# Kernel tuning notes

Hardware: AMD Instinct MI355X
Metric: run time of the kernel (lower is better)

The kernel has to match this reference:

```python
import jax, jax.numpy as jnp
import numpy as np

D_MODEL = 1024
NUM_HEADS = 16
D_K = D_MODEL // NUM_HEADS
B, S = 4, 2048


def setup_inputs() -> dict:
    key = jax.random.key(0)
    ks = jax.random.split(key, 11)
    scale = 1.0 / np.sqrt(D_MODEL)
    inp = {
        "query": jax.random.normal(ks[0], (B, S, D_MODEL), dtype=jnp.float32),
        "key": jax.random.normal(ks[1], (B, S, D_MODEL), dtype=jnp.float32),
        "value": jax.random.normal(ks[2], (B, S, D_MODEL), dtype=jnp.float32),
        "w_q": jax.random.normal(ks[3], (D_MODEL, D_MODEL), dtype=jnp.float32) * scale,
        "b_q": jnp.zeros((D_MODEL,), dtype=jnp.float32),
        "w_k": jax.random.normal(ks[4], (D_MODEL, D_MODEL), dtype=jnp.float32) * scale,
        "b_k": jnp.zeros((D_MODEL,), dtype=jnp.float32),
        "w_v": jax.random.normal(ks[5], (D_MODEL, D_MODEL), dtype=jnp.float32) * scale,
        "b_v": jnp.zeros((D_MODEL,), dtype=jnp.float32),
        "w_o": jax.random.normal(ks[6], (D_MODEL, D_MODEL), dtype=jnp.float32) * scale,
        "b_o": jnp.zeros((D_MODEL,), dtype=jnp.float32),
    }
    return inp


def reference(query, key, value, w_q, b_q, w_k, b_k, w_v, b_v, w_o, b_o):
    # Linear projections; torch Linear computes x @ W.T + b, here w_* stored as (out, in)
    def proj(x, w, b):
        y = jnp.einsum("bsd,ed->bse", x, w) + b
        # [B, S, D] -> [B, H, S, d_k]
        return y.reshape(B, S, NUM_HEADS, D_K).transpose(0, 2, 1, 3)

    Q = proj(query, w_q, b_q)
    K = proj(key, w_k, b_k)
    V = proj(value, w_v, b_v)

    scores = jnp.einsum("bhqd,bhkd->bhqk", Q, K) / jnp.sqrt(jnp.float32(D_K))
    weights = jax.nn.softmax(scores, axis=-1)
    attn = jnp.einsum("bhqk,bhkd->bhqd", weights, V)  # [B, H, S, d_k]
    attn = attn.transpose(0, 2, 1, 3).reshape(B, S, D_MODEL)
    return jnp.einsum("bsd,ed->bse", attn, w_o) + b_o
```

## Files before the change

kernel.cpp:

```cpp
#include <hip/hip_runtime.h>
#include <hip/hip_bf16.h>

#define D_MODEL 1024
#define NHEADS 16
#define DKH 64
#define BATCH 4
#define SEQ 2048
#define MROWS (BATCH*SEQ)
#define BSD ((size_t)MROWS * D_MODEL)
#define WSZ ((size_t)D_MODEL * D_MODEL)
#define LOG2E 1.4426950408889634f
#define NT (SEQ/64)

typedef __attribute__((ext_vector_type(8)))  short   s16x8;
typedef __attribute__((ext_vector_type(8)))  __bf16  bf16x8;
typedef __attribute__((ext_vector_type(4)))  __bf16  bf16x4;
typedef __attribute__((ext_vector_type(4)))  float   f32x4;
typedef __attribute__((ext_vector_type(16))) float   f32x16;

#define SWZ(row, scol) ((((int)(row)) << 6) + (((int)(scol)) ^ ((((int)(row)) & 7) << 3)))

__device__ inline short f2bf(float f) {
    __bf16 h = (__bf16)f;
    short s; __builtin_memcpy(&s, &h, 2); return s;
}

__device__ inline unsigned pk2(float a, float b) {
    unsigned r;
    asm("v_cvt_pk_bf16_f32 %0, %1, %2" : "=v"(r) : "v"(a), "v"(b));
    return r;
}
__device__ inline bf16x8 mk8(unsigned w0, unsigned w1, unsigned w2, unsigned w3) {
    union { unsigned u[4]; bf16x8 v; } x;
    x.u[0] = w0; x.u[1] = w1; x.u[2] = w2; x.u[3] = w3;
    return x.v;
}

__device__ inline void gl_lds16(const void* g, void* l) {
    __builtin_amdgcn_global_load_lds(
        (const __attribute__((address_space(1))) unsigned*)g,
        (__attribute__((address_space(3))) unsigned*)l, 16, 0, 0);
}

struct CvtPtrs { const float* src[7]; short* dst[7]; };

__global__ __launch_bounds__(256) void cvt_all(CvtPtrs p)
{
    const int bx = blockIdx.x;
    int buf, boff;
    if (bx < 3 * 4096) { buf = bx >> 12; boff = bx & 4095; }
    else { const int r = bx - 3 * 4096; buf = 3 + (r >> 9); boff = r & 511; }
    const float* __restrict__ src = p.src[buf];
    short* __restrict__ dst = p.dst[buf];
    const size_t i = ((size_t)boff * 256 + threadIdx.x) * 8;
    const float4 a = *(const float4*)(src + i);
    const float4 b = *(const float4*)(src + i + 4);
    s16x8 v;
    v[0]=f2bf(a.x); v[1]=f2bf(a.y); v[2]=f2bf(a.z); v[3]=f2bf(a.w);
    v[4]=f2bf(b.x); v[5]=f2bf(b.y); v[6]=f2bf(b.z); v[7]=f2bf(b.w);
    *(s16x8*)(dst + i) = v;
}

template<int OMODE>
__device__ __forceinline__ void gemm_body(
    const short* __restrict__ A, const short* __restrict__ W,
    const float* __restrict__ bias, void* __restrict__ Cout, float scale)
{
    __shared__ __align__(16) short As[128 * 64];
    __shared__ __align__(16) short Bs[128 * 64];
    const int t   = threadIdx.x;
    const int l   = t & 63;
    const int wid = t >> 6;
    const int g   = l >> 4, r16 = l & 15;
    const int wm  = wid >> 1, wn = wid & 1;
    const int bid = blockIdx.x + (blockIdx.y << 3);
    const int swz = (bid & 7) * 64 + (bid >> 3);
    const int n0  = (swz & 7) * 128, m0 = (swz >> 3) * 128;
    const int srow = t >> 3;
    const int scol = (t & 7) * 8;

    f32x4 acc[4][4];
    #pragma unroll
    for (int mi = 0; mi < 4; ++mi)
        #pragma unroll
        for (int ni = 0; ni < 4; ++ni)
            acc[mi][ni] = (f32x4)0.0f;

    const short* Ap = A + (size_t)(m0 + srow) * D_MODEL + scol;
    const short* Wp = W + (size_t)(n0 + srow) * D_MODEL + scol;
    short* AsW = As + wid * 512;
    short* BsW = Bs + wid * 512;

    for (int k0 = 0; k0 < D_MODEL; k0 += 64) {
        #pragma unroll
        for (int p = 0; p < 4; ++p) {
            gl_lds16(Ap + (size_t)p * 32 * D_MODEL + k0, AsW + p * 2048);
            gl_lds16(Wp + (size_t)p * 32 * D_MODEL + k0, BsW + p * 2048);
        }
        __syncthreads();
        #pragma unroll
        for (int kc = 0; kc < 2; ++kc) {
            bf16x8 a[4], b[4];
            #pragma unroll
            for (int mi = 0; mi < 4; ++mi)
                a[mi] = *(const bf16x8*)&As[(wm * 64 + mi * 16 + r16) * 64 + kc * 32 + g * 8];
            #pragma unroll
            for (int ni = 0; ni < 4; ++ni)
                b[ni] = *(const bf16x8*)&Bs[(wn * 64 + ni * 16 + r16) * 64 + kc * 32 + g * 8];
            #pragma unroll
            for (int mi = 0; mi < 4; ++mi)
                #pragma unroll
                for (int ni = 0; ni < 4; ++ni)
                    acc[mi][ni] = __builtin_amdgcn_mfma_f32_16x16x32_bf16(a[mi], b[ni], acc[mi][ni], 0, 0, 0);
        }
        __syncthreads();
    }

    #pragma unroll
    for (int mi = 0; mi < 4; ++mi)
        #pragma unroll
        for (int ni = 0; ni < 4; ++ni)
            #pragma unroll
            for (int j = 0; j < 4; ++j) {
                const int m = m0 + wm * 64 + mi * 16 + g * 4 + j;
                const int n = n0 + wn * 64 + ni * 16 + r16;
                float v = acc[mi][ni][j] + bias[n];
                if (OMODE == 1) {
                    v *= scale;
                    const size_t idx = (((size_t)((m >> 11) * NHEADS + (n >> 6)) << 11)
                                        + (size_t)(m & 2047)) * DKH + (n & 63);
                    ((short*)Cout)[idx] = f2bf(v);
                } else {
                    ((float*)Cout)[(size_t)m * D_MODEL + n] = v;
                }
            }
}

struct QkvArgs {
    const short* A[3]; const short* W[3]; const float* bias[3];
    short* out[3]; float scale[3];
};

__global__ __launch_bounds__(256, 2) void gemm_qkv(QkvArgs q) {
    const int z = blockIdx.z;
    gemm_body<1>(q.A[z], q.W[z], q.bias[z], q.out[z], q.scale[z]);
}

__global__ __launch_bounds__(256, 2) void gemm_out(
    const short* A, const short* W, const float* bias, float* C) {
    gemm_body<0>(A, W, bias, C, 1.0f);
}

__global__ __launch_bounds__(256) void transpose_v(
    const short* __restrict__ Vb, short* __restrict__ Vt)
{
    __shared__ __align__(16) short T[64][72];
    const int t  = threadIdx.x;
    const int bh = blockIdx.y;
    const int s0 = blockIdx.x * 64;
    const int row = t >> 2, cb = (t & 3) * 16;
    const short* src = Vb + ((size_t)bh * SEQ + s0 + row) * DKH + cb;
    *(s16x8*)&T[row][cb]     = *(const s16x8*)(src);
    *(s16x8*)&T[row][cb + 8] = *(const s16x8*)(src + 8);
    __syncthreads();
    const int d = t >> 2, sb = (t & 3) * 16;
    s16x8 o0, o1;
    #pragma unroll
    for (int j = 0; j < 8; ++j) { o0[j] = T[sb + j][d]; o1[j] = T[sb + 8 + j][d]; }
    short* dst = Vt + ((size_t)bh * DKH + d) * SEQ + s0 + sb;
    *(s16x8*)(dst)     = o0;
    *(s16x8*)(dst + 8) = o1;
}

__global__ __launch_bounds__(256, 3) void attn_mfma(
    const short* __restrict__ Qg, const short* __restrict__ Kg,
    const short* __restrict__ Vtg, short* __restrict__ Ab)
{
    __shared__ __align__(16) short lds[16384];
    const int t   = threadIdx.x;
    const int l   = t & 63;
    const int wid = t >> 6;
    const int l31 = l & 31, hi = l >> 5;
    const int bid = blockIdx.x + (blockIdx.y << 4);
    const int swz = (bid & 7) * 128 + (bid >> 3);
    const int bh  = swz >> 4, b = bh >> 4, h = bh & 15;
    const int q0  = (swz & 15) << 7;
    const int wq0 = wid * 32;
    const int srow = t >> 3, scol = (t & 7) * 8;
    const int kr = t >> 2, kcb = (t & 3) * 16;

    #pragma unroll
    for (int p = 0; p < 4; ++p) {
        const int row = srow + p * 32;
        *(s16x8*)&lds[SWZ(row, scol)] =
            *(const s16x8*)&Qg[((size_t)bh * SEQ + q0 + row) * DKH + scol];
    }
    const short* Kbase = Kg  + (size_t)bh * SEQ * DKH;
    const short* Vbase = Vtg + (size_t)bh * DKH * SEQ;
    s16x8 kpf0 = *(const s16x8*)&Kbase[(size_t)kr * DKH + kcb];
    s16x8 kpf1 = *(const s16x8*)&Kbase[(size_t)kr * DKH + kcb + 8];
    s16x8 vpf0 = *(const s16x8*)&Vbase[(size_t)kr * SEQ + kcb];
    s16x8 vpf1 = *(const s16x8*)&Vbase[(size_t)kr * SEQ + kcb + 8];
    __syncthreads();

    bf16x8 bq[4];
    #pragma unroll
    for (int kc = 0; kc < 4; ++kc)
        bq[kc] = *(const bf16x8*)&lds[SWZ(wq0 + l31, kc * 16 + hi * 8)];

    *(s16x8*)&lds[8192  + SWZ(kr, kcb)]     = kpf0;
    *(s16x8*)&lds[8192  + SWZ(kr, kcb + 8)] = kpf1;
    *(s16x8*)&lds[12288 + SWZ(kr, kcb)]     = vpf0;
    *(s16x8*)&lds[12288 + SWZ(kr, kcb + 8)] = vpf1;
    kpf0 = *(const s16x8*)&Kbase[(size_t)(64 + kr) * DKH + kcb];
    kpf1 = *(const s16x8*)&Kbase[(size_t)(64 + kr) * DKH + kcb + 8];
    vpf0 = *(const s16x8*)&Vbase[(size_t)kr * SEQ + 64 + kcb];
    vpf1 = *(const s16x8*)&Vbase[(size_t)kr * SEQ + 64 + kcb + 8];
    __syncthreads();

    f32x16 o0 = (f32x16)0.0f, o1 = (f32x16)0.0f;
    float m_r = -1e30f, l_r = 0.0f;

    for (int kt = 0; kt < NT; ++kt) {
        const int cur = kt & 1;
        const int KO = cur ? 0     : 8192;
        const int VO = cur ? 4096  : 12288;
        const int KN = cur ? 8192  : 0;
        const int VN = cur ? 12288 : 4096;
        if (kt + 1 < NT) {
            *(s16x8*)&lds[KN + SWZ(kr, kcb)]     = kpf0;
            *(s16x8*)&lds[KN + SWZ(kr, kcb + 8)] = kpf1;
            *(s16x8*)&lds[VN + SWZ(kr, kcb)]     = vpf0;
            *(s16x8*)&lds[VN + SWZ(kr, kcb + 8)] = vpf1;
        }
        if (kt + 2 < NT) {
            kpf0 = *(const s16x8*)&Kbase[(size_t)((kt + 2) * 64 + kr) * DKH + kcb];
            kpf1 = *(const s16x8*)&Kbase[(size_t)((kt + 2) * 64 + kr) * DKH + kcb + 8];
            vpf0 = *(const s16x8*)&Vbase[(size_t)kr * SEQ + (kt + 2) * 64 + kcb];
            vpf1 = *(const s16x8*)&Vbase[(size_t)kr * SEQ + (kt + 2) * 64 + kcb + 8];
        }

        f32x16 s0 = (f32x16)0.0f, s1 = (f32x16)0.0f;
        __builtin_amdgcn_s_setprio(1);
        #pragma unroll
        for (int kc = 0; kc < 4; ++kc) {
            const bf16x8 ak0 = *(const bf16x8*)&lds[KO + SWZ(l31,      kc * 16 + hi * 8)];
            const bf16x8 ak1 = *(const bf16x8*)&lds[KO + SWZ(32 + l31, kc * 16 + hi * 8)];
            s0 = __builtin_amdgcn_mfma_f32_32x32x16_bf16(ak0, bq[kc], s0, 0, 0, 0);
            s1 = __builtin_amdgcn_mfma_f32_32x32x16_bf16(ak1, bq[kc], s1, 0, 0, 0);
        }
        __builtin_amdgcn_s_setprio(0);

        float mx = s0[0];
        #pragma unroll
        for (int r = 1; r < 16; ++r) mx = fmaxf(mx, s0[r]);
        #pragma unroll
        for (int r = 0; r < 16; ++r) mx = fmaxf(mx, s1[r]);
        mx = fmaxf(mx, __shfl_xor(mx, 32));
        if (__any(mx > m_r + 8.0f)) {
            const float mnew = fmaxf(m_r, mx);
            const float resc = __builtin_amdgcn_exp2f(m_r - mnew);
            m_r = mnew;
            l_r *= resc;
            #pragma unroll
            for (int r = 0; r < 16; ++r) { o0[r] *= resc; o1[r] *= resc; }
        }
        float sum = 0.0f;
        #pragma unroll
        for (int r = 0; r < 16; ++r) {
            const float p = __builtin_amdgcn_exp2f(s0[r] - m_r);
            s0[r] = p; sum += p;
        }
        #pragma unroll
        for (int r = 0; r < 16; ++r) {
            const float p = __builtin_amdgcn_exp2f(s1[r] - m_r);
            s1[r] = p; sum += p;
        }
        l_r += sum;

        bf16x8 bp[4];
        {
            unsigned a0 = pk2(s0[0], s0[1]),  b0 = pk2(s0[4],  s0[5]);
            unsigned a1 = pk2(s0[2], s0[3]),  b1 = pk2(s0[6],  s0[7]);
            asm("v_permlane32_swap_b32 %0, %1" : "+v"(a0), "+v"(b0));
            asm("v_permlane32_swap_b32 %0, %1" : "+v"(a1), "+v"(b1));
            bp[0] = mk8(a0, a1, b0, b1);
            unsigned a2 = pk2(s0[8], s0[9]),   b2 = pk2(s0[12], s0[13]);
            unsigned a3 = pk2(s0[10], s0[11]), b3 = pk2(s0[14], s0[15]);
            asm("v_permlane32_swap_b32 %0, %1" : "+v"(a2), "+v"(b2));
            asm("v_permlane32_swap_b32 %0, %1" : "+v"(a3), "+v"(b3));
            bp[1] = mk8(a2, a3, b2, b3);
        }
        {
            unsigned a0 = pk2(s1[0], s1[1]),  b0 = pk2(s1[4],  s1[5]);
            unsigned a1 = pk2(s1[2], s1[3]),  b1 = pk2(s1[6],  s1[7]);
            asm("v_permlane32_swap_b32 %0, %1" : "+v"(a0), "+v"(b0));
            asm("v_permlane32_swap_b32 %0, %1" : "+v"(a1), "+v"(b1));
            bp[2] = mk8(a0, a1, b0, b1);
            unsigned a2 = pk2(s1[8], s1[9]),   b2 = pk2(s1[12], s1[13]);
            unsigned a3 = pk2(s1[10], s1[11]), b3 = pk2(s1[14], s1[15]);
            asm("v_permlane32_swap_b32 %0, %1" : "+v"(a2), "+v"(b2));
            asm("v_permlane32_swap_b32 %0, %1" : "+v"(a3), "+v"(b3));
            bp[3] = mk8(a2, a3, b2, b3);
        }

        __builtin_amdgcn_s_setprio(1);
        #pragma unroll
        for (int ks = 0; ks < 4; ++ks) {
            const bf16x8 av0 = *(const bf16x8*)&lds[VO + SWZ(l31,      ks * 16 + hi * 8)];
            const bf16x8 av1 = *(const bf16x8*)&lds[VO + SWZ(32 + l31, ks * 16 + hi * 8)];
            o0 = __builtin_amdgcn_mfma_f32_32x32x16_bf16(av0, bp[ks], o0, 0, 0, 0);
            o1 = __builtin_amdgcn_mfma_f32_32x32x16_bf16(av1, bp[ks], o1, 0, 0, 0);
        }
        __builtin_amdgcn_s_setprio(0);

        __syncthreads();
    }

    const float lt = l_r + __shfl_xor(l_r, 32);
    const float inv = 1.0f / lt;
    const int q = q0 + wq0 + l31;
    short* Op = Ab + ((size_t)b * SEQ + q) * D_MODEL + h * DKH;
    #pragma unroll
    for (int rr = 0; rr < 4; ++rr) {
        bf16x4 ov;
        ov[0] = (__bf16)(o0[rr*4+0] * inv); ov[1] = (__bf16)(o0[rr*4+1] * inv);
        ov[2] = (__bf16)(o0[rr*4+2] * inv); ov[3] = (__bf16)(o0[rr*4+3] * inv);
        *(bf16x4*)&Op[rr * 8 + hi * 4] = ov;
        bf16x4 ow;
        ow[0] = (__bf16)(o1[rr*4+0] * inv); ow[1] = (__bf16)(o1[rr*4+1] * inv);
        ow[2] = (__bf16)(o1[rr*4+2] * inv); ow[3] = (__bf16)(o1[rr*4+3] * inv);
        *(bf16x4*)&Op[32 + rr * 8 + hi * 4] = ow;
    }
}

extern "C" void kernel_launch(void* const* d_in, const int* in_sizes, int n_in,
                              void* d_out, int out_size, void* d_ws, size_t ws_size,
                              hipStream_t stream) {
    const float* q_in = (const float*)d_in[0];
    const float* k_in = (const float*)d_in[1];
    const float* v_in = (const float*)d_in[2];
    const float* w_q  = (const float*)d_in[3];
    const float* b_q  = (const float*)d_in[4];
    const float* w_k  = (const float*)d_in[5];
    const float* b_k  = (const float*)d_in[6];
    const float* w_v  = (const float*)d_in[7];
    const float* b_v  = (const float*)d_in[8];
    const float* w_o  = (const float*)d_in[9];
    const float* b_o  = (const float*)d_in[10];
    float* out = (float*)d_out;

    short* ws = (short*)d_ws;
    short* Qc = ws;
    short* Kc = ws + BSD;
    short* Vc = ws + 2 * BSD;
    short* Wq = ws + 3 * BSD;
    short* Wk = Wq + WSZ;
    short* Wv = Wk + WSZ;
    short* Wo = Wv + WSZ;
    short* Qb = ws + 3 * BSD + 4 * WSZ;
    short* Kb = Qb + BSD;
    short* Vb = Kb + BSD;
    short* Vt = Qc;
    short* Ab = Kc;

    dim3 blk(256);

    CvtPtrs cp;
    cp.src[0] = q_in; cp.dst[0] = Qc;
    cp.src[1] = k_in; cp.dst[1] = Kc;
    cp.src[2] = v_in; cp.dst[2] = Vc;
    cp.src[3] = w_q;  cp.dst[3] = Wq;
    cp.src[4] = w_k;  cp.dst[4] = Wk;
    cp.src[5] = w_v;  cp.dst[5] = Wv;
    cp.src[6] = w_o;  cp.dst[6] = Wo;
    cvt_all<<<dim3(3 * 4096 + 4 * 512), blk, 0, stream>>>(cp);

    QkvArgs qa;
    qa.A[0] = Qc; qa.W[0] = Wq; qa.bias[0] = b_q; qa.out[0] = Qb; qa.scale[0] = 0.125f * LOG2E;
    qa.A[1] = Kc; qa.W[1] = Wk; qa.bias[1] = b_k; qa.out[1] = Kb; qa.scale[1] = 1.0f;
    qa.A[2] = Vc; qa.W[2] = Wv; qa.bias[2] = b_v; qa.out[2] = Vb; qa.scale[2] = 1.0f;
    gemm_qkv<<<dim3(D_MODEL / 128, MROWS / 128, 3), blk, 0, stream>>>(qa);

    transpose_v<<<dim3(SEQ / 64, BATCH * NHEADS), blk, 0, stream>>>(Vb, Vt);

    attn_mfma<<<dim3(SEQ / 128, BATCH * NHEADS), blk, 0, stream>>>(Qb, Kb, Vt, Ab);

    gemm_out<<<dim3(D_MODEL / 128, MROWS / 128), blk, 0, stream>>>(Ab, Wo, b_o, out);
}
```

Baseline: 218.0 us.

## Shrink attention key tile to 32 to cut LDS and raise occupancy

Halves the key/value tile per iteration from 64 to 32 keys, shrinking LDS double buffers and dropping one score accumulator. It adds a new swizzle for the narrower V tile and raises launch bounds to 4 blocks per CU. The aim is lower register and LDS pressure so more waves can hide latency. The cost is twice as many loop iterations, each with its own barrier and softmax max/rescale check, and smaller MFMA batches per step.

```diff
diff --git a/kernel.cpp b/kernel.cpp
--- a/kernel.cpp
+++ b/kernel.cpp
@@ -10,7 +10,7 @@
 #define BSD ((size_t)MROWS * D_MODEL)
 #define WSZ ((size_t)D_MODEL * D_MODEL)
 #define LOG2E 1.4426950408889634f
-#define NT (SEQ/64)
+#define NT2 (SEQ/32)
 
 typedef __attribute__((ext_vector_type(8)))  short   s16x8;
 typedef __attribute__((ext_vector_type(8)))  __bf16  bf16x8;
@@ -19,6 +19,7 @@
 typedef __attribute__((ext_vector_type(16))) float   f32x16;
 
 #define SWZ(row, scol) ((((int)(row)) << 6) + (((int)(scol)) ^ ((((int)(row)) & 7) << 3)))
+#define SWZV(row, scol) ((((int)(row)) << 5) + (((int)(scol)) ^ (((((int)(row)) >> 1) & 3) << 3)))
 
 __device__ inline short f2bf(float f) {
     __bf16 h = (__bf16)f;
@@ -172,11 +173,11 @@
     *(s16x8*)(dst + 8) = o1;
 }
 
-__global__ __launch_bounds__(256, 3) void attn_mfma(
+__global__ __launch_bounds__(256, 4) void attn_mfma(
     const short* __restrict__ Qg, const short* __restrict__ Kg,
     const short* __restrict__ Vtg, short* __restrict__ Ab)
 {
-    __shared__ __align__(16) short lds[16384];
+    __shared__ __align__(16) short lds[12288];
     const int t   = threadIdx.x;
     const int l   = t & 63;
     const int wid = t >> 6;
@@ -186,21 +187,21 @@
     const int bh  = swz >> 4, b = bh >> 4, h = bh & 15;
     const int q0  = (swz & 15) << 7;
     const int wq0 = wid * 32;
-    const int srow = t >> 3, scol = (t & 7) * 8;
-    const int kr = t >> 2, kcb = (t & 3) * 16;
+    const int qrow = t >> 3, qcol = (t & 7) * 8;
+    const int vrow = t >> 2, vcol = (t & 3) * 8;
 
     #pragma unroll
     for (int p = 0; p < 4; ++p) {
-        const int row = srow + p * 32;
-        *(s16x8*)&lds[SWZ(row, scol)] =
-            *(const s16x8*)&Qg[((size_t)bh * SEQ + q0 + row) * DKH + scol];
+        const int row = qrow + p * 32;
+        *(s16x8*)&lds[SWZ(row, qcol)] =
+            *(const s16x8*)&Qg[((size_t)bh * SEQ + q0 + row) * DKH + qcol];
     }
     const short* Kbase = Kg  + (size_t)bh * SEQ * DKH;
     const short* Vbase = Vtg + (size_t)bh * DKH * SEQ;
-    s16x8 kpf0 = *(const s16x8*)&Kbase[(size_t)kr * DKH + kcb];
-    s16x8 kpf1 = *(const s16x8*)&Kbase[(size_t)kr * DKH + kcb + 8];
-    s16x8 vpf0 = *(const s16x8*)&Vbase[(size_t)kr * SEQ + kcb];
-    s16x8 vpf1 = *(const s16x8*)&Vbase[(size_t)kr * SEQ + kcb + 8];
+    const int koff = qrow * DKH + qcol;
+    const int voff = vrow * SEQ + vcol;
+    s16x8 kpf = *(const s16x8*)&Kbase[koff];
+    s16x8 vpf = *(const s16x8*)&Vbase[voff];
     __syncthreads();
 
     bf16x8 bq[4];
@@ -208,54 +209,43 @@
     for (int kc = 0; kc < 4; ++kc)
         bq[kc] = *(const bf16x8*)&lds[SWZ(wq0 + l31, kc * 16 + hi * 8)];
 
-    *(s16x8*)&lds[8192  + SWZ(kr, kcb)]     = kpf0;
-    *(s16x8*)&lds[8192  + SWZ(kr, kcb + 8)] = kpf1;
-    *(s16x8*)&lds[12288 + SWZ(kr, kcb)]     = vpf0;
-    *(s16x8*)&lds[12288 + SWZ(kr, kcb + 8)] = vpf1;
-    kpf0 = *(const s16x8*)&Kbase[(size_t)(64 + kr) * DKH + kcb];
-    kpf1 = *(const s16x8*)&Kbase[(size_t)(64 + kr) * DKH + kcb + 8];
-    vpf0 = *(const s16x8*)&Vbase[(size_t)kr * SEQ + 64 + kcb];
-    vpf1 = *(const s16x8*)&Vbase[(size_t)kr * SEQ + 64 + kcb + 8];
+    *(s16x8*)&lds[8192  + SWZ(qrow, qcol)]  = kpf;
+    *(s16x8*)&lds[10240 + SWZV(vrow, vcol)] = vpf;
+    kpf = *(const s16x8*)&Kbase[koff + 2048];
+    vpf = *(const s16x8*)&Vbase[voff + 32];
     __syncthreads();
 
     f32x16 o0 = (f32x16)0.0f, o1 = (f32x16)0.0f;
     float m_r = -1e30f, l_r = 0.0f;
 
-    for (int kt = 0; kt < NT; ++kt) {
+    for (int kt = 0; kt < NT2; ++kt) {
         const int cur = kt & 1;
         const int KO = cur ? 0     : 8192;
-        const int VO = cur ? 4096  : 12288;
+        const int VO = cur ? 2048  : 10240;
         const int KN = cur ? 8192  : 0;
-        const int VN = cur ? 12288 : 4096;
-        if (kt + 1 < NT) {
-            *(s16x8*)&lds[KN + SWZ(kr, kcb)]     = kpf0;
-            *(s16x8*)&lds[KN + SWZ(kr, kcb + 8)] = kpf1;
-            *(s16x8*)&lds[VN + SWZ(kr, kcb)]     = vpf0;
-            *(s16x8*)&lds[VN + SWZ(kr, kcb + 8)] = vpf1;
-        }
-        if (kt + 2 < NT) {
-            kpf0 = *(const s16x8*)&Kbase[(size_t)((kt + 2) * 64 + kr) * DKH + kcb];
-            kpf1 = *(const s16x8*)&Kbase[(size_t)((kt + 2) * 64 + kr) * DKH + kcb + 8];
-            vpf0 = *(const s16x8*)&Vbase[(size_t)kr * SEQ + (kt + 2) * 64 + kcb];
-            vpf1 = *(const s16x8*)&Vbase[(size_t)kr * SEQ + (kt + 2) * 64 + kcb + 8];
-        }
-
-        f32x16 s0 = (f32x16)0.0f, s1 = (f32x16)0.0f;
+        const int VN = cur ? 10240 : 2048;
+        if (kt + 1 < NT2) {
+            *(s16x8*)&lds[KN + SWZ(qrow, qcol)]  = kpf;
+            *(s16x8*)&lds[VN + SWZV(vrow, vcol)] = vpf;
+        }
+        if (kt + 2 < NT2) {
+            kpf = *(const s16x8*)&Kbase[koff + (kt + 2) * 2048];
+            vpf = *(const s16x8*)&Vbase[voff + (kt + 2) * 32];
+        }
+
+        f32x16 s = (f32x16)0.0f;
         __builtin_amdgcn_s_setprio(1);
         #pragma unroll
         for (int kc = 0; kc < 4; ++kc) {
-            const bf16x8 ak0 = *(const bf16x8*)&lds[KO + SWZ(l31,      kc * 16 + hi * 8)];
-            const bf16x8 ak1 = *(const bf16x8*)&lds[KO + SWZ(32 + l31, kc * 16 + hi * 8)];
-            s0 = __builtin_amdgcn_mfma_f32_32x32x16_bf16(ak0, bq[kc], s0, 0, 0, 0);
-            s1 = __builtin_amdgcn_mfma_f32_32x32x16_bf16(ak1, bq[kc], s1, 0, 0, 0);
+            const bf16x8 ak = *(const bf16x8*)&lds[KO + SWZ(l31, kc * 16 + hi * 8)];
+            s = __builtin_amdgcn_mfma_f32_32x32x16_bf16(ak, bq[kc], s, 0, 0, 0);
         }
         __builtin_amdgcn_s_setprio(0);
 
-        float mx = s0[0];
-        #pragma unroll
-        for (int r = 1; r < 16; ++r) mx = fmaxf(mx, s0[r]);
-        #pragma unroll
-        for (int r = 0; r < 16; ++r) mx = fmaxf(mx, s1[r]);
+        float mx = fmaxf(fmaxf(fmaxf(s[0], s[1]), fmaxf(s[2], s[3])),
+                         fmaxf(fmaxf(s[4], s[5]), fmaxf(s[6], s[7])));
+        mx = fmaxf(mx, fmaxf(fmaxf(fmaxf(s[8], s[9]), fmaxf(s[10], s[11])),
+                             fmaxf(fmaxf(s[12], s[13]), fmaxf(s[14], s[15]))));
         mx = fmaxf(mx, __shfl_xor(mx, 32));
         if (__any(mx > m_r + 8.0f)) {
             const float mnew = fmaxf(m_r, mx);
@@ -268,49 +258,35 @@
         float sum = 0.0f;
         #pragma unroll
         for (int r = 0; r < 16; ++r) {
-            const float p = __builtin_amdgcn_exp2f(s0[r] - m_r);
-            s0[r] = p; sum += p;
-        }
-        #pragma unroll
-        for (int r = 0; r < 16; ++r) {
-            const float p = __builtin_amdgcn_exp2f(s1[r] - m_r);
-            s1[r] = p; sum += p;
+            const float p = __builtin_amdgcn_exp2f(s[r] - m_r);
+            s[r] = p; sum += p;
         }
         l_r += sum;
 
-        bf16x8 bp[4];
+        bf16x8 bp0, bp1;
         {
-            unsigned a0 = pk2(s0[0], s0[1]),  b0 = pk2(s0[4],  s0[5]);
-            unsigned a1 = pk2(s0[2], s0[3]),  b1 = pk2(s0[6],  s0[7]);
+            unsigned a0 = pk2(s[0], s[1]),  b0 = pk2(s[4],  s[5]);
+            unsigned a1 = pk2(s[2], s[3]),  b1 = pk2(s[6],  s[7]);
             asm("v_permlane32_swap_b32 %0, %1" : "+v"(a0), "+v"(b0));
             asm("v_permlane32_swap_b32 %0, %1" : "+v"(a1), "+v"(b1));
-            bp[0] = mk8(a0, a1, b0, b1);
-            unsigned a2 = pk2(s0[8], s0[9]),   b2 = pk2(s0[12], s0[13]);
-            unsigned a3 = pk2(s0[10], s0[11]), b3 = pk2(s0[14], s0[15]);
+            bp0 = mk8(a0, a1, b0, b1);
+            unsigned a2 = pk2(s[8], s[9]),   b2 = pk2(s[12], s[13]);
+            unsigned a3 = pk2(s[10], s[11]), b3 = pk2(s[14], s[15]);
             asm("v_permlane32_swap_b32 %0, %1" : "+v"(a2), "+v"(b2));
             asm("v_permlane32_swap_b32 %0, %1" : "+v"(a3), "+v"(b3));
-            bp[1] = mk8(a2, a3, b2, b3);
-        }
+            bp1 = mk8(a2, a3, b2, b3);
+        }
+
+        __builtin_amdgcn_s_setprio(1);
         {
-            unsigned a0 = pk2(s1[0], s1[1]),  b0 = pk2(s1[4],  s1[5]);
-            unsigned a1 = pk2(s1[2], s1[3]),  b1 = pk2(s1[6],  s1[7]);
-            asm("v_permlane32_swap_b32 %0, %1" : "+v"(a0), "+v"(b0));
-            asm("v_permlane32_swap_b32 %0, %1" : "+v"(a1), "+v"(b1));
-            bp[2] = mk8(a0, a1, b0, b1);
-            unsigned a2 = pk2(s1[8], s1[9]),   b2 = pk2(s1[12], s1[13]);
-            unsigned a3 = pk2(s1[10], s1[11]), b3 = pk2(s1[14], s1[15]);
-            asm("v_permlane32_swap_b32 %0, %1" : "+v"(a2), "+v"(b2));
-            asm("v_permlane32_swap_b32 %0, %1" : "+v"(a3), "+v"(b3));
-            bp[3] = mk8(a2, a3, b2, b3);
-        }
-
-        __builtin_amdgcn_s_setprio(1);
-        #pragma unroll
-        for (int ks = 0; ks < 4; ++ks) {
-            const bf16x8 av0 = *(const bf16x8*)&lds[VO + SWZ(l31,      ks * 16 + hi * 8)];
-            const bf16x8 av1 = *(const bf16x8*)&lds[VO + SWZ(32 + l31, ks * 16 + hi * 8)];
-            o0 = __builtin_amdgcn_mfma_f32_32x32x16_bf16(av0, bp[ks], o0, 0, 0, 0);
-            o1 = __builtin_amdgcn_mfma_f32_32x32x16_bf16(av1, bp[ks], o1, 0, 0, 0);
+            const bf16x8 av00 = *(const bf16x8*)&lds[VO + SWZV(l31,      hi * 8)];
+            const bf16x8 av01 = *(const bf16x8*)&lds[VO + SWZV(32 + l31, hi * 8)];
+            o0 = __builtin_amdgcn_mfma_f32_32x32x16_bf16(av00, bp0, o0, 0, 0, 0);
+            o1 = __builtin_amdgcn_mfma_f32_32x32x16_bf16(av01, bp0, o1, 0, 0, 0);
+            const bf16x8 av10 = *(const bf16x8*)&lds[VO + SWZV(l31,      16 + hi * 8)];
+            const bf16x8 av11 = *(const bf16x8*)&lds[VO + SWZV(32 + l31, 16 + hi * 8)];
+            o0 = __builtin_amdgcn_mfma_f32_32x32x16_bf16(av10, bp1, o0, 0, 0, 0);
+            o1 = __builtin_amdgcn_mfma_f32_32x32x16_bf16(av11, bp1, o1, 0, 0, 0);
         }
         __builtin_amdgcn_s_setprio(0);
 
```

Measured after the change: 223.3 us. +2.4%, slower.
